# Kernel optimization log

Hardware: AMD Instinct MI355X
Metric: run time of the kernel (lower is better)

The kernel has to match this reference:

```python
import jax, jax.numpy as jnp
import numpy as np
from jax import lax

BITS = 8  # w_p = a_p = 8 (HAWQ int8)

def _round_ste(x):
    # straight-through round (quant-aware training semantics)
    return x + lax.stop_gradient(jnp.round(x) - x)

def _quant_act(x):
    # QuantAct: symmetric per-tensor activation fake-quant; returns (quantized x, scale)
    n = 2.0 ** (BITS - 1) - 1.0
    sf = jnp.maximum(jnp.max(jnp.abs(x)) / n, 1e-8)
    q = jnp.clip(_round_ste(x / sf), -n, n)
    return q * sf, sf

def _quant_conv(x, w, b, pre_sf, stride, pad):
    # QuantConv2d: per-output-channel symmetric weight quant, integer conv on
    # x/pre_sf with rounded weights, rescale by pre_sf * w_sf. Bias quantized at
    # combined scale. Returns (float output, w_sf) for scale propagation.
    n = 2.0 ** (BITS - 1) - 1.0
    w_sf = jnp.maximum(jnp.max(jnp.abs(w), axis=(1, 2, 3)) / n, 1e-8)
    w_int = _round_ste(w / w_sf[:, None, None, None])
    b_sf = w_sf * pre_sf
    b_int = _round_ste(b / b_sf)
    y = lax.conv_general_dilated(x / pre_sf, w_int, (stride, stride),
                                 [(pad, pad), (pad, pad)],
                                 dimension_numbers=('NCHW', 'OIHW', 'NCHW'))
    return (y + b_int[None, :, None, None]) * b_sf[None, :, None, None], w_sf

def _bn(x, g, b, m, v, eps=1e-5):
    # BatchNorm2d in eval mode (running stats), folded into scale/shift
    inv = g / jnp.sqrt(v + eps)
    return x * inv[None, :, None, None] + (b - m * inv)[None, :, None, None]

def _quant_linear(x, w, b, pre_sf):
    # QuantLinear: per-output-row symmetric weight quant
    n = 2.0 ** (BITS - 1) - 1.0
    w_sf = jnp.maximum(jnp.max(jnp.abs(w), axis=1) / n, 1e-8)
    w_int = _round_ste(w / w_sf[:, None])
    b_sf = w_sf * pre_sf
    b_int = _round_ste(b / b_sf)
    return ((x / pre_sf) @ w_int.T + b_int[None, :]) * b_sf[None, :]

def _forward(x, w0, b0, g0, bb0, m0, v0, w1, b1, g1, bb1, m1, v1,
             w2, b2, g2, bb2, m2, v2, w3, b3, g3, bb3, m3, v3,
             w4, b4, g4, bb4, m4, v4, wd, bd):
    x, psf = _quant_act(x)
    x, _ = _quant_conv(x, w0, b0, psf, 1, 1)   # [B,32,32,32]
    x = _bn(x, g0, bb0, m0, v0)
    x, psf = _quant_act(x)
    x, _ = _quant_conv(x, w1, b1, psf, 1, 0)   # 1x1 -> [B,4,32,32]
    x = _bn(x, g1, bb1, m1, v1)
    x, psf = _quant_act(x)
    x, _ = _quant_conv(x, w2, b2, psf, 2, 1)   # [B,32,16,16]
    x = _bn(x, g2, bb2, m2, v2)
    x, psf = _quant_act(x)
    x, _ = _quant_conv(x, w3, b3, psf, 2, 1)   # [B,32,8,8]
    x = _bn(x, g3, bb3, m3, v3)
    x, psf = _quant_act(x)
    x, _ = _quant_conv(x, w4, b4, psf, 1, 1)   # [B,32,8,8]
    x = _bn(x, g4, bb4, m4, v4)
    x, psf = _quant_act(x)
    x = x.reshape(-1, 2048)                    # 32*8*8 = 2048
    x = _quant_linear(x, wd, bd, psf)          # [B,10]
    return jax.nn.softmax(x, axis=0)           # dim=0 as in original module

def setup_inputs() -> dict:
    key = jax.random.key(0)
    ks = jax.random.split(key, 40)
    B = 1024
    inp = {"x": jax.random.normal(ks[0], (B, 3, 32, 32), jnp.float32)}
    conv_shapes = [(32, 3, 3, 3), (4, 32, 1, 1), (32, 4, 3, 3), (32, 32, 3, 3), (32, 32, 3, 3)]
    for i, s in enumerate(conv_shapes):
        c = s[0]
        inp[f"w{i}"] = jax.random.normal(ks[1 + i], s, jnp.float32) * 0.1
        inp[f"b{i}"] = jax.random.normal(ks[6 + i], (c,), jnp.float32) * 0.01
        inp[f"g{i}"] = 1.0 + 0.1 * jax.random.normal(ks[11 + i], (c,), jnp.float32)
        inp[f"bb{i}"] = 0.1 * jax.random.normal(ks[16 + i], (c,), jnp.float32)
        inp[f"m{i}"] = 0.1 * jax.random.normal(ks[21 + i], (c,), jnp.float32)
        inp[f"v{i}"] = 0.5 + jax.random.uniform(ks[26 + i], (c,), jnp.float32)
    inp["wd"] = jax.random.normal(ks[31], (10, 2048), jnp.float32) * 0.05
    inp["bd"] = jnp.zeros((10,), jnp.float32)
    return inp

def reference(x, w0, b0, g0, bb0, m0, v0, w1, b1, g1, bb1, m1, v1,
              w2, b2, g2, bb2, m2, v2, w3, b3, g3, bb3, m3, v3,
              w4, b4, g4, bb4, m4, v4, wd, bd):
    return _forward(x, w0, b0, g0, bb0, m0, v0, w1, b1, g1, bb1, m1, v1,
                    w2, b2, g2, bb2, m2, v2, w3, b3, g3, bb3, m3, v3,
                    w4, b4, g4, bb4, m4, v4, wd, bd)
```

## Files before the change

### kernel.cpp

```cpp
#include <hip/hip_runtime.h>

#define DI __device__ __forceinline__

constexpr int OFF_W0KT = 384;
constexpr int OFF_W0P  = 1248;
constexpr int OFF_W1I  = 2144;
constexpr int OFF_W2KT = 2272;
constexpr int OFF_W3T  = 3424;
constexpr int OFF_W4T  = 13792;
constexpr int OFF_WDI  = 24160;
constexpr int OFF_WSF0 = 44640;
constexpr int OFF_BNS0 = 44672;
constexpr int OFF_BNB0 = 44704;
constexpr int OFF_WSF1 = 44736;
constexpr int OFF_BNS1 = 44740;
constexpr int OFF_BNB1 = 44744;
constexpr int OFF_WSF2 = 44748;
constexpr int OFF_BNS2 = 44780;
constexpr int OFF_BNB2 = 44812;
constexpr int OFF_WSF3 = 44844;
constexpr int OFF_BNS3 = 44876;
constexpr int OFF_BNB3 = 44908;
constexpr int OFF_WSF4 = 44940;
constexpr int OFF_BNS4 = 44972;
constexpr int OFF_BNB4 = 45004;
constexpr int OFF_WSFD = 45036;
constexpr int OFF_LOG  = 45056;
constexpr int OFF_ACT  = 55296;
constexpr long ACT_A_OFF = OFF_ACT;
constexpr long ACT_B_OFF = OFF_ACT + 8388608L;

DI float quantm(float x, float rsf) {
    float q = rintf(x * rsf);
    return fminf(fmaxf(q, -127.0f), 127.0f);
}
DI float get_sf(const unsigned* umax, int slot) {
    const unsigned* p = umax + slot * 64;
    unsigned m = 0u;
    #pragma unroll
    for (int i = 0; i < 64; ++i) m = m > p[i] ? m : p[i];
    return fmaxf(__uint_as_float(m) / 127.0f, 1e-8f);
}
DI void block_max_atomic(float v, unsigned* dst) {
    __shared__ float redm_[4];
    #pragma unroll
    for (int o = 32; o; o >>= 1) v = fmaxf(v, __shfl_down(v, o, 64));
    int wid = threadIdx.x >> 6;
    if ((threadIdx.x & 63) == 0) redm_[wid] = v;
    __syncthreads();
    if (threadIdx.x == 0) {
        int nw = blockDim.x >> 6;
        float m = redm_[0];
        for (int i = 1; i < nw; ++i) m = fmaxf(m, redm_[i]);
        atomicMax(dst + (blockIdx.x & 63), __float_as_uint(m));
    }
}

struct PrepEntry {
    const float *w, *g, *bb, *m, *v;
    float *wsf, *dst, *dst2, *bns, *bnb;
    int K; int has_bn; int mode;
};
struct PrepAll { PrepEntry e[6]; unsigned* umax; };

__global__ __launch_bounds__(256) void k_prep_all(PrepAll pa) {
    int blk = blockIdx.x;
    if (blk == 142) {
        for (int i = threadIdx.x; i < 384; i += 256) pa.umax[i] = 0u;
        return;
    }
    int layer, oc;
    if      (blk < 32)  { layer = 0; oc = blk; }
    else if (blk < 36)  { layer = 1; oc = blk - 32; }
    else if (blk < 68)  { layer = 2; oc = blk - 36; }
    else if (blk < 100) { layer = 3; oc = blk - 68; }
    else if (blk < 132) { layer = 4; oc = blk - 100; }
    else                { layer = 5; oc = blk - 132; }
    PrepEntry a = pa.e[layer];
    const float* wr = a.w + (long)oc * a.K;
    float mx = 0.f;
    for (int i = threadIdx.x; i < a.K; i += 256) mx = fmaxf(mx, fabsf(wr[i]));
    __shared__ float red[4];
    __shared__ float s_sf;
    #pragma unroll
    for (int o = 32; o; o >>= 1) mx = fmaxf(mx, __shfl_down(mx, o, 64));
    if ((threadIdx.x & 63) == 0) red[threadIdx.x >> 6] = mx;
    __syncthreads();
    if (threadIdx.x == 0) {
        float t = fmaxf(fmaxf(red[0], red[1]), fmaxf(red[2], red[3]));
        t = fmaxf(t / 127.0f, 1e-8f);
        a.wsf[oc] = t; s_sf = t;
        if (a.has_bn) {
            float inv = a.g[oc] / sqrtf(a.v[oc] + 1e-5f);
            a.bns[oc] = inv;
            a.bnb[oc] = a.bb[oc] - a.m[oc] * inv;
        }
    }
    __syncthreads();
    float sf = s_sf;
    for (int i = threadIdx.x; i < a.K; i += 256) {
        float q = rintf(wr[i] / sf);
        if (a.mode == 0) {
            a.dst[(long)oc * a.K + i] = q;
        } else if (a.mode == 1) {
            a.dst[i * 32 + oc] = q;
        } else if (a.mode == 2) {
            a.dst[i * 32 + oc] = q;
            a.dst2[oc * 28 + i] = q;
        } else {
            int ph = i / 72, kk = i - ph * 72;
            a.dst[ph * 2592 + kk * 36 + oc] = q;
        }
    }
    if (a.mode == 2 && threadIdx.x == 0) a.dst2[oc * 28 + 27] = 0.f;
}

__global__ __launch_bounds__(256) void k_absmax(const float4* __restrict__ x, int n4, unsigned* dst) {
    float m = 0.f;
    for (int i = blockIdx.x * blockDim.x + threadIdx.x; i < n4; i += gridDim.x * blockDim.x) {
        float4 t = x[i];
        m = fmaxf(m, fmaxf(fmaxf(fabsf(t.x), fabsf(t.y)), fmaxf(fabsf(t.z), fabsf(t.w))));
    }
    block_max_atomic(m, dst);
}

__global__ __launch_bounds__(256) void k_conv0maxN(
    const float* __restrict__ x, const float* __restrict__ w0kt,
    const float* __restrict__ wsf0, const float* __restrict__ bias0,
    const float* __restrict__ bns0, const float* __restrict__ bnb0,
    const unsigned* __restrict__ umax, unsigned* __restrict__ mout) {
    __shared__ float tile[3 * 18 * 36];
    __shared__ float wlds[27 * 32];
    __shared__ float As[32], Cs[32];
    const int b  = blockIdx.x >> 1;
    const int r0 = (blockIdx.x & 1) * 16;
    const int tid = threadIdx.x;
    const float sfx = get_sf(umax, 0);
    const float rsfx = 1.0f / sfx;
    if (tid < 32) {
        int oc = tid;
        float bsf = wsf0[oc] * sfx;
        float bint = rintf(bias0[oc] / bsf);
        float a = bsf * bns0[oc];
        As[oc] = a;
        Cs[oc] = fmaf(bint, a, bnb0[oc]);
    }
    for (int i = tid; i < 1944; i += 256) tile[i] = 0.f;
    if (tid < 216) ((float4*)wlds)[tid] = ((const float4*)w0kt)[tid];
    __syncthreads();
    const float* xb = x + (long)b * 3072;
    for (int i = tid; i < 1728; i += 256) {
        int ci = i / 576, rem = i - ci * 576;
        int rr = rem >> 5, cc = rem & 31;
        int gr = r0 - 1 + rr;
        if ((unsigned)gr < 32u)
            tile[ci * 648 + rr * 36 + cc + 1] = quantm(xb[ci * 1024 + gr * 32 + cc], rsfx);
    }
    __syncthreads();
    const int oc0  = (tid >> 5) * 4;
    const int pxg  = tid & 31;
    const int row  = pxg >> 1;
    const int wcol = (pxg & 1) * 16;
    float acc[4][16];
    #pragma unroll
    for (int o = 0; o < 4; ++o)
        #pragma unroll
        for (int p = 0; p < 16; ++p) acc[o][p] = 0.f;
    #pragma unroll 1
    for (int kk = 0; kk < 9; ++kk) {
        int ci = kk / 3, ky = kk - ci * 3;
        const float* rp = tile + ci * 648 + (row + ky) * 36 + wcol;
        float wn[20];
        #pragma unroll
        for (int d = 0; d < 5; ++d) *(float4*)&wn[4 * d] = *(const float4*)&rp[4 * d];
        #pragma unroll
        for (int kx = 0; kx < 3; ++kx) {
            float4 wv = *(const float4*)&wlds[(kk * 3 + kx) * 32 + oc0];
            const float* wf = &wv.x;
            #pragma unroll
            for (int o = 0; o < 4; ++o)
                #pragma unroll
                for (int p = 0; p < 16; ++p)
                    acc[o][p] = fmaf(wn[p + kx], wf[o], acc[o][p]);
        }
    }
    float lmax = 0.f;
    #pragma unroll
    for (int o = 0; o < 4; ++o) {
        float A = As[oc0 + o], C = Cs[oc0 + o];
        #pragma unroll
        for (int p = 0; p < 16; ++p)
            lmax = fmaxf(lmax, fabsf(fmaf(acc[o][p], A, C)));
    }
    block_max_atomic(lmax, mout);
}

__global__ __launch_bounds__(256) void k_conv01n(
    const float* __restrict__ x, const float* __restrict__ w0p,
    const float* __restrict__ wsf0, const float* __restrict__ bias0,
    const float* __restrict__ bns0, const float* __restrict__ bnb0,
    const float* __restrict__ w1i,
    const float* __restrict__ wsf1, const float* __restrict__ bias1,
    const float* __restrict__ bns1, const float* __restrict__ bnb1,
    const unsigned* __restrict__ umax, unsigned* __restrict__ mout,
    float* __restrict__ out) {
    __shared__ float tile[3672];
    __shared__ float wls0[896];
    __shared__ float wls1[128];
    __shared__ float Aq[32], Cq[32];
    __shared__ float A1s[4], C1s[4];
    const int b   = blockIdx.x;
    const int tid = threadIdx.x;
    const float sfx = get_sf(umax, 0);
    const float rsfx = 1.0f / sfx;
    const float sf1 = get_sf(umax, 1);
    const float rsf1 = 1.0f / sf1;
    if (tid < 32) {
        int oc = tid;
        float bsf = wsf0[oc] * sfx;
        float bint = rintf(bias0[oc] / bsf);
        float a = bsf * bns0[oc];
        float c = fmaf(bint, a, bnb0[oc]);
        Aq[oc] = a * rsf1;
        Cq[oc] = c * rsf1;
    }
    if (tid >= 64 && tid < 68) {
        int oc = tid - 64;
        float bsf = wsf1[oc] * sf1;
        float bint = rintf(bias1[oc] / bsf);
        float a = bsf * bns1[oc];
        A1s[oc] = a;
        C1s[oc] = fmaf(bint, a, bnb1[oc]);
    }
    for (int i = tid; i < 3672; i += 256) tile[i] = 0.f;
    if (tid < 224) ((float4*)wls0)[tid] = ((const float4*)w0p)[tid];
    if (tid >= 128 && tid < 256) {
        int j = tid - 128;
        wls1[(j & 31) * 4 + (j >> 5)] = w1i[j];
    }
    __syncthreads();
    const float* xb = x + (long)b * 3072;
    for (int i = tid; i < 3072; i += 256) {
        int ci = i >> 10, px = i & 1023;
        int iy = px >> 5, ix = px & 31;
        tile[ci * 1224 + (iy + 1) * 36 + (ix + 1)] = quantm(xb[i], rsfx);
    }
    __syncthreads();
    const int h   = tid >> 3;
    const int w0c = (tid & 7) * 4;
    float win[3][3][6];
    #pragma unroll
    for (int ci = 0; ci < 3; ++ci)
        #pragma unroll
        for (int ky = 0; ky < 3; ++ky) {
            const int base = ci * 1224 + (h + ky) * 36 + w0c;
            *(float4*)&win[ci][ky][0] = *(const float4*)&tile[base];
            *(float2*)&win[ci][ky][4] = *(const float2*)&tile[base + 4];
        }
    float acc1[4][4];
    #pragma unroll
    for (int o = 0; o < 4; ++o)
        #pragma unroll
        for (int p = 0; p < 4; ++p) acc1[o][p] = 0.f;
    #pragma unroll 1
    for (int oc = 0; oc < 32; ++oc) {
        float wreg[28];
        const float4* wp4 = (const float4*)&wls0[oc * 28];
        #pragma unroll
        for (int d = 0; d < 7; ++d) *(float4*)&wreg[4 * d] = wp4[d];
        float a0 = 0.f, a1 = 0.f, a2 = 0.f, a3 = 0.f;
        #pragma unroll
        for (int ci = 0; ci < 3; ++ci)
            #pragma unroll
            for (int ky = 0; ky < 3; ++ky)
                #pragma unroll
                for (int kx = 0; kx < 3; ++kx) {
                    float wv = wreg[ci * 9 + ky * 3 + kx];
                    a0 = fmaf(win[ci][ky][kx + 0], wv, a0);
                    a1 = fmaf(win[ci][ky][kx + 1], wv, a1);
                    a2 = fmaf(win[ci][ky][kx + 2], wv, a2);
                    a3 = fmaf(win[ci][ky][kx + 3], wv, a3);
                }
        float A = Aq[oc], C = Cq[oc];
        float q0 = fminf(fmaxf(rintf(fmaf(a0, A, C)), -127.0f), 127.0f);
        float q1 = fminf(fmaxf(rintf(fmaf(a1, A, C)), -127.0f), 127.0f);
        float q2 = fminf(fmaxf(rintf(fmaf(a2, A, C)), -127.0f), 127.0f);
        float q3 = fminf(fmaxf(rintf(fmaf(a3, A, C)), -127.0f), 127.0f);
        const float4 w1v = *(const float4*)&wls1[oc * 4];
        acc1[0][0] = fmaf(q0, w1v.x, acc1[0][0]); acc1[0][1] = fmaf(q1, w1v.x, acc1[0][1]);
        acc1[0][2] = fmaf(q2, w1v.x, acc1[0][2]); acc1[0][3] = fmaf(q3, w1v.x, acc1[0][3]);
        acc1[1][0] = fmaf(q0, w1v.y, acc1[1][0]); acc1[1][1] = fmaf(q1, w1v.y, acc1[1][1]);
        acc1[1][2] = fmaf(q2, w1v.y, acc1[1][2]); acc1[1][3] = fmaf(q3, w1v.y, acc1[1][3]);
        acc1[2][0] = fmaf(q0, w1v.z, acc1[2][0]); acc1[2][1] = fmaf(q1, w1v.z, acc1[2][1]);
        acc1[2][2] = fmaf(q2, w1v.z, acc1[2][2]); acc1[2][3] = fmaf(q3, w1v.z, acc1[2][3]);
        acc1[3][0] = fmaf(q0, w1v.w, acc1[3][0]); acc1[3][1] = fmaf(q1, w1v.w, acc1[3][1]);
        acc1[3][2] = fmaf(q2, w1v.w, acc1[3][2]); acc1[3][3] = fmaf(q3, w1v.w, acc1[3][3]);
    }
    float lmax = 0.f;
    float* ob = out + (long)b * 4096 + h * 32 + w0c;
    #pragma unroll
    for (int o = 0; o < 4; ++o) {
        float y0 = fmaf(acc1[o][0], A1s[o], C1s[o]);
        float y1 = fmaf(acc1[o][1], A1s[o], C1s[o]);
        float y2 = fmaf(acc1[o][2], A1s[o], C1s[o]);
        float y3 = fmaf(acc1[o][3], A1s[o], C1s[o]);
        lmax = fmaxf(lmax, fmaxf(fmaxf(fabsf(y0), fabsf(y1)), fmaxf(fabsf(y2), fabsf(y3))));
        float4 r4; r4.x = y0; r4.y = y1; r4.z = y2; r4.w = y3;
        *(float4*)&ob[o * 1024] = r4;
    }
    block_max_atomic(lmax, mout);
}

__global__ __launch_bounds__(256) void k_conv2c(
    const float* __restrict__ inp, const float* __restrict__ w2kt,
    const float* __restrict__ wsf, const float* __restrict__ bias,
    const float* __restrict__ bns, const float* __restrict__ bnb,
    const unsigned* __restrict__ umax, unsigned* __restrict__ mout,
    float* __restrict__ out) {
    __shared__ float tile[4 * 34 * 36];
    __shared__ float wlds[36 * 32];
    __shared__ float As[32], Cs[32];
    const int tid = threadIdx.x;
    const float sf = get_sf(umax, 2);
    const float rsf = 1.0f / sf;
    if (tid < 32) {
        int oc = tid;
        float bsf = wsf[oc] * sf;
        float bint = rintf(bias[oc] / bsf);
        float a = bsf * bns[oc];
        As[oc] = a;
        Cs[oc] = fmaf(bint, a, bnb[oc]);
    }
    for (int i = tid; i < 4896; i += 256) tile[i] = 0.f;
    for (int i = tid; i < 288; i += 256) ((float4*)wlds)[i] = ((const float4*)w2kt)[i];
    __syncthreads();
    const float* ib = inp + (long)blockIdx.x * 4096;
    for (int i = tid; i < 4096; i += 256) {
        int ci = i >> 10, px = i & 1023;
        int iy = px >> 5, ix = px & 31;
        tile[ci * 1224 + (iy + 1) * 36 + (ix + 1)] = quantm(ib[i], rsf);
    }
    __syncthreads();
    const int oc0 = (tid >> 6) * 8;
    const int pxq = tid & 63;
    const int h = pxq >> 2, c = pxq & 3;
    float acc[8][4];
    #pragma unroll
    for (int k = 0; k < 8; ++k)
        #pragma unroll
        for (int p = 0; p < 4; ++p) acc[k][p] = 0.f;
    #pragma unroll 1
    for (int ci = 0; ci < 4; ++ci) {
        #pragma unroll
        for (int ky = 0; ky < 3; ++ky) {
            const float* rp = tile + ci * 1224 + (2 * h + ky) * 36 + 8 * c;
            float wn[12];
            #pragma unroll
            for (int d = 0; d < 3; ++d) *(float4*)&wn[4 * d] = *(const float4*)&rp[4 * d];
            #pragma unroll
            for (int kx = 0; kx < 3; ++kx) {
                const float* wp = &wlds[(ci * 9 + ky * 3 + kx) * 32 + oc0];
                float4 wa = *(const float4*)&wp[0];
                float4 wb = *(const float4*)&wp[4];
                float wf[8] = {wa.x, wa.y, wa.z, wa.w, wb.x, wb.y, wb.z, wb.w};
                #pragma unroll
                for (int k = 0; k < 8; ++k)
                    #pragma unroll
                    for (int p = 0; p < 4; ++p)
                        acc[k][p] = fmaf(wn[2 * p + kx], wf[k], acc[k][p]);
            }
        }
    }
    float lmax = 0.f;
    float* ob = out + (long)blockIdx.x * 8192;
    #pragma unroll
    for (int k = 0; k < 8; ++k) {
        int oc = oc0 + k;
        float A = As[oc], C = Cs[oc];
        float4 r;
        float* rp = &r.x;
        #pragma unroll
        for (int p = 0; p < 4; ++p) {
            float y = fmaf(acc[k][p], A, C);
            rp[p] = y;
            lmax = fmaxf(lmax, fabsf(y));
        }
        *(float4*)&ob[oc * 256 + h * 16 + c * 4] = r;
    }
    block_max_atomic(lmax, mout);
}

template<int HIN, int S>
__global__ __launch_bounds__(256) void k_conv34c(
    const float* __restrict__ inp, const float* __restrict__ wt,
    const float* __restrict__ wsf, const float* __restrict__ bias,
    const float* __restrict__ bns, const float* __restrict__ bnb,
    const unsigned* __restrict__ umax, int slot, unsigned* __restrict__ mout,
    float* __restrict__ out) {
    constexpr int ROWS = HIN + 2;
    constexpr int RS   = (S == 2) ? 20 : 12;
    constexpr int TI   = 8 * ROWS * RS;
    constexpr int PIX  = HIN * HIN;
    constexpr int NELT = 8 * PIX;
    constexpr int WINW = S + 3;
    __shared__ float tile[TI];
    __shared__ float wlds[72 * 36];
    __shared__ float As[32], Cs[32];
    const int tid = threadIdx.x;
    const int ocg = tid >> 5;
    const int pxq = tid & 31;
    const int h = pxq >> 2, c = pxq & 3;
    const float sf = get_sf(umax, slot);
    const float rsf = 1.0f / sf;
    if (tid < 32) {
        int oc = tid;
        float bsf = wsf[oc] * sf;
        float bint = rintf(bias[oc] / bsf);
        float a = bsf * bns[oc];
        As[oc] = a;
        Cs[oc] = fmaf(bint, a, bnb[oc]);
    }
    for (int i = tid; i < TI; i += 256) tile[i] = 0.f;
    float acc[4][2];
    #pragma unroll
    for (int k = 0; k < 4; ++k) { acc[k][0] = 0.f; acc[k][1] = 0.f; }
    const float* ib = inp + (long)blockIdx.x * 32 * PIX;
    const float4* wt4 = (const float4*)wt;
    for (int ph = 0; ph < 4; ++ph) {
        __syncthreads();
        for (int i = tid; i < NELT; i += 256) {
            int ci = i / PIX;
            int px = i - ci * PIX;
            int iy = px / HIN, ix = px & (HIN - 1);
            tile[ci * (ROWS * RS) + (iy + 1) * RS + (ix + 1)] =
                quantm(ib[(long)(ph * 8 + ci) * PIX + px], rsf);
        }
        for (int i = tid; i < 648; i += 256) ((float4*)wlds)[i] = wt4[ph * 648 + i];
        __syncthreads();
        #pragma unroll 2
        for (int ci = 0; ci < 8; ++ci) {
            float win[3][WINW];
            #pragma unroll
            for (int ky = 0; ky < 3; ++ky) {
                const int base = ci * (ROWS * RS) + (S * h + ky) * RS + S * 2 * c;
                if (S == 2) {
                    *(float4*)&win[ky][0] = *(const float4*)&tile[base];
                    win[ky][4] = tile[base + 4];
                } else {
                    *(float2*)&win[ky][0] = *(const float2*)&tile[base];
                    *(float2*)&win[ky][2] = *(const float2*)&tile[base + 2];
                }
            }
            #pragma unroll
            for (int ky = 0; ky < 3; ++ky)
                #pragma unroll
                for (int kx = 0; kx < 3; ++kx) {
                    int j = ky * 3 + kx;
                    float4 wv = *(const float4*)&wlds[(ci * 9 + j) * 36 + ocg * 4];
                    float x0 = win[ky][kx], x1 = win[ky][S + kx];
                    acc[0][0] = fmaf(x0, wv.x, acc[0][0]); acc[0][1] = fmaf(x1, wv.x, acc[0][1]);
                    acc[1][0] = fmaf(x0, wv.y, acc[1][0]); acc[1][1] = fmaf(x1, wv.y, acc[1][1]);
                    acc[2][0] = fmaf(x0, wv.z, acc[2][0]); acc[2][1] = fmaf(x1, wv.z, acc[2][1]);
                    acc[3][0] = fmaf(x0, wv.w, acc[3][0]); acc[3][1] = fmaf(x1, wv.w, acc[3][1]);
                }
        }
    }
    float lmax = 0.f;
    #pragma unroll
    for (int k = 0; k < 4; ++k) {
        int oc = ocg * 4 + k;
        float A = As[oc], C = Cs[oc];
        float y0 = fmaf(acc[k][0], A, C);
        float y1 = fmaf(acc[k][1], A, C);
        lmax = fmaxf(lmax, fmaxf(fabsf(y0), fabsf(y1)));
        float2 r2; r2.x = y0; r2.y = y1;
        *(float2*)&out[((long)blockIdx.x * 32 + oc) * 64 + h * 8 + c * 2] = r2;
    }
    block_max_atomic(lmax, mout);
}

__global__ __launch_bounds__(256) void k_fc(
    const float* __restrict__ act, const float* __restrict__ wdi,
    const float* __restrict__ wsfd, const float* __restrict__ bd,
    const unsigned* __restrict__ umax, float* __restrict__ logits) {
    int b = blockIdx.x;
    float sf = get_sf(umax, 5);
    float rsf = 1.0f / sf;
    const float* ab = act + (long)b * 2048;
    float acc[10];
    #pragma unroll
    for (int c = 0; c < 10; ++c) acc[c] = 0.f;
    #pragma unroll
    for (int k = 0; k < 8; ++k) {
        int j = threadIdx.x + 256 * k;
        float q = quantm(ab[j], rsf);
        #pragma unroll
        for (int c = 0; c < 10; ++c) acc[c] = fmaf(q, wdi[c * 2048 + j], acc[c]);
    }
    #pragma unroll
    for (int c = 0; c < 10; ++c)
        #pragma unroll
        for (int o = 32; o; o >>= 1) acc[c] += __shfl_down(acc[c], o, 64);
    __shared__ float red[4][10];
    int wid = threadIdx.x >> 6;
    if ((threadIdx.x & 63) == 0)
        #pragma unroll
        for (int c = 0; c < 10; ++c) red[wid][c] = acc[c];
    __syncthreads();
    if (threadIdx.x < 10) {
        int c = threadIdx.x;
        float s = red[0][c] + red[1][c] + red[2][c] + red[3][c];
        float bsf = wsfd[c] * sf;
        float bint = rintf(bd[c] / bsf);
        logits[b * 10 + c] = (s + bint) * bsf;
    }
}

__global__ __launch_bounds__(256) void k_softmax(const float* __restrict__ logits, float* __restrict__ out) {
    int c = blockIdx.x;
    float v0 = logits[(threadIdx.x +   0) * 10 + c];
    float v1 = logits[(threadIdx.x + 256) * 10 + c];
    float v2 = logits[(threadIdx.x + 512) * 10 + c];
    float v3 = logits[(threadIdx.x + 768) * 10 + c];
    float mx = fmaxf(fmaxf(v0, v1), fmaxf(v2, v3));
    __shared__ float redm[4];
    __shared__ float reds[4];
    #pragma unroll
    for (int o = 32; o; o >>= 1) mx = fmaxf(mx, __shfl_down(mx, o, 64));
    if ((threadIdx.x & 63) == 0) redm[threadIdx.x >> 6] = mx;
    __syncthreads();
    mx = fmaxf(fmaxf(redm[0], redm[1]), fmaxf(redm[2], redm[3]));
    float e0 = expf(v0 - mx), e1 = expf(v1 - mx), e2 = expf(v2 - mx), e3 = expf(v3 - mx);
    float s = (e0 + e1) + (e2 + e3);
    #pragma unroll
    for (int o = 32; o; o >>= 1) s += __shfl_down(s, o, 64);
    if ((threadIdx.x & 63) == 0) reds[threadIdx.x >> 6] = s;
    __syncthreads();
    s = reds[0] + reds[1] + reds[2] + reds[3];
    out[(threadIdx.x +   0) * 10 + c] = e0 / s;
    out[(threadIdx.x + 256) * 10 + c] = e1 / s;
    out[(threadIdx.x + 512) * 10 + c] = e2 / s;
    out[(threadIdx.x + 768) * 10 + c] = e3 / s;
}

extern "C" void kernel_launch(void* const* d_in, const int* in_sizes, int n_in,
                              void* d_out, int out_size, void* d_ws, size_t ws_size,
                              hipStream_t stream) {
    (void)in_sizes; (void)n_in; (void)out_size; (void)ws_size;
    const float* x = (const float*)d_in[0];
    const float *w[5], *bia[5], *g[5], *bb[5], *m[5], *v[5];
    for (int i = 0; i < 5; ++i) {
        w[i]   = (const float*)d_in[1 + 6 * i + 0];
        bia[i] = (const float*)d_in[1 + 6 * i + 1];
        g[i]   = (const float*)d_in[1 + 6 * i + 2];
        bb[i]  = (const float*)d_in[1 + 6 * i + 3];
        m[i]   = (const float*)d_in[1 + 6 * i + 4];
        v[i]   = (const float*)d_in[1 + 6 * i + 5];
    }
    const float* wd = (const float*)d_in[31];
    const float* bd = (const float*)d_in[32];
    float* ws = (float*)d_ws;
    unsigned* umax = (unsigned*)ws;
    float* out = (float*)d_out;

    float* w0kt = ws + OFF_W0KT;
    float* w0p  = ws + OFF_W0P;
    float* w1i  = ws + OFF_W1I;
    float* w2kt = ws + OFF_W2KT;
    float* w3t  = ws + OFF_W3T;
    float* w4t  = ws + OFF_W4T;
    float* wdi  = ws + OFF_WDI;
    float* wsf0 = ws + OFF_WSF0; float* bns0 = ws + OFF_BNS0; float* bnb0 = ws + OFF_BNB0;
    float* wsf1 = ws + OFF_WSF1; float* bns1 = ws + OFF_BNS1; float* bnb1 = ws + OFF_BNB1;
    float* wsf2 = ws + OFF_WSF2; float* bns2 = ws + OFF_BNS2; float* bnb2 = ws + OFF_BNB2;
    float* wsf3 = ws + OFF_WSF3; float* bns3 = ws + OFF_BNS3; float* bnb3 = ws + OFF_BNB3;
    float* wsf4 = ws + OFF_WSF4; float* bns4 = ws + OFF_BNS4; float* bnb4 = ws + OFF_BNB4;
    float* wsfd = ws + OFF_WSFD;
    float* logits = ws + OFF_LOG;
    float* actA = ws + ACT_A_OFF;
    float* actB = ws + ACT_B_OFF;

    PrepAll pa;
    pa.umax = umax;
    const float* ww[6] = {w[0], w[1], w[2], w[3], w[4], wd};
    float* wsfp[6] = {wsf0, wsf1, wsf2, wsf3, wsf4, wsfd};
    float* dstp[6] = {w0kt, w1i, w2kt, w3t, w4t, wdi};
    float* dst2p[6] = {w0p, nullptr, nullptr, nullptr, nullptr, nullptr};
    float* bnsp[6] = {bns0, bns1, bns2, bns3, bns4, nullptr};
    float* bnbp[6] = {bnb0, bnb1, bnb2, bnb3, bnb4, nullptr};
    int Ks[6]   = {27, 32, 36, 288, 288, 2048};
    int modes[6] = {2, 0, 1, 3, 3, 0};
    for (int i = 0; i < 6; ++i) {
        pa.e[i].w = ww[i];
        pa.e[i].g = (i < 5) ? g[i] : nullptr;
        pa.e[i].bb = (i < 5) ? bb[i] : nullptr;
        pa.e[i].m = (i < 5) ? m[i] : nullptr;
        pa.e[i].v = (i < 5) ? v[i] : nullptr;
        pa.e[i].wsf = wsfp[i];
        pa.e[i].dst = dstp[i];
        pa.e[i].dst2 = dst2p[i];
        pa.e[i].bns = bnsp[i];
        pa.e[i].bnb = bnbp[i];
        pa.e[i].K = Ks[i];
        pa.e[i].has_bn = (i < 5) ? 1 : 0;
        pa.e[i].mode = modes[i];
    }

    hipLaunchKernelGGL(k_prep_all, dim3(143), dim3(256), 0, stream, pa);
    hipLaunchKernelGGL(k_absmax, dim3(1024), dim3(256), 0, stream,
                       (const float4*)x, 1024 * 3 * 32 * 32 / 4, umax + 0 * 64);
    hipLaunchKernelGGL(k_conv0maxN, dim3(2048), dim3(256), 0, stream,
                       x, w0kt, wsf0, bia[0], bns0, bnb0, umax, umax + 1 * 64);
    hipLaunchKernelGGL(k_conv01n, dim3(1024), dim3(256), 0, stream,
                       x, w0p, wsf0, bia[0], bns0, bnb0,
                       w1i, wsf1, bia[1], bns1, bnb1, umax, umax + 2 * 64, actB);
    hipLaunchKernelGGL(k_conv2c, dim3(1024), dim3(256), 0, stream,
                       actB, w2kt, wsf2, bia[2], bns2, bnb2, umax, umax + 3 * 64, actA);
    hipLaunchKernelGGL((k_conv34c<16, 2>), dim3(1024), dim3(256), 0, stream,
                       actA, w3t, wsf3, bia[3], bns3, bnb3, umax, 3, umax + 4 * 64, actB);
    hipLaunchKernelGGL((k_conv34c<8, 1>),  dim3(1024), dim3(256), 0, stream,
                       actB, w4t, wsf4, bia[4], bns4, bnb4, umax, 4, umax + 5 * 64, actA);
    hipLaunchKernelGGL(k_fc, dim3(1024), dim3(256), 0, stream, actA, wdi, wsfd, bd, umax, logits);
    hipLaunchKernelGGL(k_softmax, dim3(10), dim3(256), 0, stream, logits, out);
}
```

Measured before the change: 176.0 us.

## Process two images per block in conv3/conv4 with four outputs per thread

The conv3/conv4 kernel now handles two images per 256-thread block, with half the threads assigned to each image. Each thread computes four output pixels instead of two for its four output channels. This raises weight reuse per LDS load, loads the input window with wider float4 reads, and halves the grid and the number of per-block atomic max reductions. In exchange it doubles the input tile in shared memory and adds accumulator registers, which may lower occupancy.

```diff
diff --git a/kernel.cpp b/kernel.cpp
--- a/kernel.cpp
+++ b/kernel.cpp
@@ -391,7 +391,7 @@
 }
 
 template<int HIN, int S>
-__global__ __launch_bounds__(256) void k_conv34c(
+__global__ __launch_bounds__(256) void k_conv34d(
     const float* __restrict__ inp, const float* __restrict__ wt,
     const float* __restrict__ wsf, const float* __restrict__ bias,
     const float* __restrict__ bns, const float* __restrict__ bnb,
@@ -401,15 +401,19 @@
     constexpr int RS   = (S == 2) ? 20 : 12;
     constexpr int TI   = 8 * ROWS * RS;
     constexpr int PIX  = HIN * HIN;
-    constexpr int NELT = 8 * PIX;
-    constexpr int WINW = S + 3;
-    __shared__ float tile[TI];
-    __shared__ float wlds[72 * 36];
+    constexpr int PSH  = (HIN == 16) ? 8 : 6;
+    constexpr int HSH  = (HIN == 16) ? 4 : 3;
+    constexpr int NELT = 2 * 8 * PIX;
+    constexpr int WINW = (S == 2) ? 12 : 8;
+    constexpr int ND   = (S == 2) ? 3 : 2;
+    __shared__ float tile[2 * TI];
+    __shared__ float wlds[2592];
     __shared__ float As[32], Cs[32];
-    const int tid = threadIdx.x;
-    const int ocg = tid >> 5;
-    const int pxq = tid & 31;
-    const int h = pxq >> 2, c = pxq & 3;
+    const int tid  = threadIdx.x;
+    const int imgl = tid >> 7;
+    const int ocg  = (tid >> 4) & 7;
+    const int pxq  = tid & 15;
+    const int h = pxq >> 1, c = pxq & 1;
     const float sf = get_sf(umax, slot);
     const float rsf = 1.0f / sf;
     if (tid < 32) {
@@ -420,36 +424,36 @@
         As[oc] = a;
         Cs[oc] = fmaf(bint, a, bnb[oc]);
     }
-    for (int i = tid; i < TI; i += 256) tile[i] = 0.f;
-    float acc[4][2];
-    #pragma unroll
-    for (int k = 0; k < 4; ++k) { acc[k][0] = 0.f; acc[k][1] = 0.f; }
-    const float* ib = inp + (long)blockIdx.x * 32 * PIX;
+    for (int i = tid; i < 2 * TI; i += 256) tile[i] = 0.f;
+    float acc[4][4];
+    #pragma unroll
+    for (int k = 0; k < 4; ++k)
+        #pragma unroll
+        for (int p = 0; p < 4; ++p) acc[k][p] = 0.f;
+    const float* ib = inp + (long)blockIdx.x * 2 * 32 * PIX;
     const float4* wt4 = (const float4*)wt;
     for (int ph = 0; ph < 4; ++ph) {
         __syncthreads();
         for (int i = tid; i < NELT; i += 256) {
-            int ci = i / PIX;
-            int px = i - ci * PIX;
-            int iy = px / HIN, ix = px & (HIN - 1);
-            tile[ci * (ROWS * RS) + (iy + 1) * RS + (ix + 1)] =
-                quantm(ib[(long)(ph * 8 + ci) * PIX + px], rsf);
+            int im = i >> (PSH + 3);
+            int ci = (i >> PSH) & 7;
+            int px = i & (PIX - 1);
+            int iy = px >> HSH, ix = px & (HIN - 1);
+            tile[im * TI + ci * (ROWS * RS) + (iy + 1) * RS + (ix + 1)] =
+                quantm(ib[(long)((im * 32 + ph * 8 + ci) << PSH) + px], rsf);
         }
         for (int i = tid; i < 648; i += 256) ((float4*)wlds)[i] = wt4[ph * 648 + i];
         __syncthreads();
+        const int tbo = imgl * TI;
         #pragma unroll 2
         for (int ci = 0; ci < 8; ++ci) {
             float win[3][WINW];
             #pragma unroll
             for (int ky = 0; ky < 3; ++ky) {
-                const int base = ci * (ROWS * RS) + (S * h + ky) * RS + S * 2 * c;
-                if (S == 2) {
-                    *(float4*)&win[ky][0] = *(const float4*)&tile[base];
-                    win[ky][4] = tile[base + 4];
-                } else {
-                    *(float2*)&win[ky][0] = *(const float2*)&tile[base];
-                    *(float2*)&win[ky][2] = *(const float2*)&tile[base + 2];
-                }
+                const int base = tbo + ci * (ROWS * RS) + (S * h + ky) * RS + S * 4 * c;
+                #pragma unroll
+                for (int d = 0; d < ND; ++d)
+                    *(float4*)&win[ky][4 * d] = *(const float4*)&tile[base + 4 * d];
             }
             #pragma unroll
             for (int ky = 0; ky < 3; ++ky)
@@ -457,24 +461,34 @@
                 for (int kx = 0; kx < 3; ++kx) {
                     int j = ky * 3 + kx;
                     float4 wv = *(const float4*)&wlds[(ci * 9 + j) * 36 + ocg * 4];
-                    float x0 = win[ky][kx], x1 = win[ky][S + kx];
+                    float x0 = win[ky][S * 0 + kx];
+                    float x1 = win[ky][S * 1 + kx];
+                    float x2 = win[ky][S * 2 + kx];
+                    float x3 = win[ky][S * 3 + kx];
                     acc[0][0] = fmaf(x0, wv.x, acc[0][0]); acc[0][1] = fmaf(x1, wv.x, acc[0][1]);
+                    acc[0][2] = fmaf(x2, wv.x, acc[0][2]); acc[0][3] = fmaf(x3, wv.x, acc[0][3]);
                     acc[1][0] = fmaf(x0, wv.y, acc[1][0]); acc[1][1] = fmaf(x1, wv.y, acc[1][1]);
+                    acc[1][2] = fmaf(x2, wv.y, acc[1][2]); acc[1][3] = fmaf(x3, wv.y, acc[1][3]);
                     acc[2][0] = fmaf(x0, wv.z, acc[2][0]); acc[2][1] = fmaf(x1, wv.z, acc[2][1]);
+                    acc[2][2] = fmaf(x2, wv.z, acc[2][2]); acc[2][3] = fmaf(x3, wv.z, acc[2][3]);
                     acc[3][0] = fmaf(x0, wv.w, acc[3][0]); acc[3][1] = fmaf(x1, wv.w, acc[3][1]);
+                    acc[3][2] = fmaf(x2, wv.w, acc[3][2]); acc[3][3] = fmaf(x3, wv.w, acc[3][3]);
                 }
         }
     }
     float lmax = 0.f;
+    long imgg = (long)blockIdx.x * 2 + imgl;
     #pragma unroll
     for (int k = 0; k < 4; ++k) {
         int oc = ocg * 4 + k;
         float A = As[oc], C = Cs[oc];
         float y0 = fmaf(acc[k][0], A, C);
         float y1 = fmaf(acc[k][1], A, C);
-        lmax = fmaxf(lmax, fmaxf(fabsf(y0), fabsf(y1)));
-        float2 r2; r2.x = y0; r2.y = y1;
-        *(float2*)&out[((long)blockIdx.x * 32 + oc) * 64 + h * 8 + c * 2] = r2;
+        float y2 = fmaf(acc[k][2], A, C);
+        float y3 = fmaf(acc[k][3], A, C);
+        lmax = fmaxf(lmax, fmaxf(fmaxf(fabsf(y0), fabsf(y1)), fmaxf(fabsf(y2), fabsf(y3))));
+        float4 r4; r4.x = y0; r4.y = y1; r4.z = y2; r4.w = y3;
+        *(float4*)&out[(imgg * 32 + oc) * 64 + h * 8 + c * 4] = r4;
     }
     block_max_atomic(lmax, mout);
 }
@@ -616,9 +630,9 @@
                        w1i, wsf1, bia[1], bns1, bnb1, umax, umax + 2 * 64, actB);
     hipLaunchKernelGGL(k_conv2c, dim3(1024), dim3(256), 0, stream,
                        actB, w2kt, wsf2, bia[2], bns2, bnb2, umax, umax + 3 * 64, actA);
-    hipLaunchKernelGGL((k_conv34c<16, 2>), dim3(1024), dim3(256), 0, stream,
+    hipLaunchKernelGGL((k_conv34d<16, 2>), dim3(512), dim3(256), 0, stream,
                        actA, w3t, wsf3, bia[3], bns3, bnb3, umax, 3, umax + 4 * 64, actB);
-    hipLaunchKernelGGL((k_conv34c<8, 1>),  dim3(1024), dim3(256), 0, stream,
+    hipLaunchKernelGGL((k_conv34d<8, 1>),  dim3(512), dim3(256), 0, stream,
                        actB, w4t, wsf4, bia[4], bns4, bnb4, umax, 4, umax + 5 * 64, actA);
     hipLaunchKernelGGL(k_fc, dim3(1024), dim3(256), 0, stream, actA, wdi, wsfd, bd, umax, logits);
     hipLaunchKernelGGL(k_softmax, dim3(10), dim3(256), 0, stream, logits, out);
```

After: 164.6 us. 1.07x faster.
